# Optimization experiments

Measured on AMD Instinct MI355X. Metric: run time of the kernel, lower is better.

## Reference

```python
import jax, jax.numpy as jnp
import numpy as np

N_USER = 100000
N_ITEM = 100000
N_EDGE = 1600000
HID = 64
IN_U = 128
IN_I = 64
N_LAYERS = 2


def setup_inputs() -> dict:
    key = jax.random.key(0)
    ks = jax.random.split(key, 12)
    s = 0.05
    return {
        "x_user": jax.random.normal(ks[0], (N_USER, IN_U), jnp.float32),
        "x_item": jax.random.normal(ks[1], (N_ITEM, IN_I), jnp.float32),
        "edge_ui": jax.random.randint(ks[2], (2, N_EDGE), 0, N_USER),  # row0 src(user), row1 dst(item)
        "edge_iu": jax.random.randint(ks[3], (2, N_EDGE), 0, N_ITEM),  # row0 src(item), row1 dst(user)
        "Wu": jax.random.normal(ks[4], (IN_U, HID), jnp.float32) * s,
        "bu": jnp.zeros((HID,), jnp.float32),
        "Wi": jax.random.normal(ks[5], (IN_I, HID), jnp.float32) * s,
        "bi": jnp.zeros((HID,), jnp.float32),
        "Wl": jax.random.normal(ks[6], (N_LAYERS, 2, HID, HID), jnp.float32) * s,
        "bl": jnp.zeros((N_LAYERS, 2, HID), jnp.float32),
        "Wr": jax.random.normal(ks[7], (N_LAYERS, 2, HID, HID), jnp.float32) * s,
    }


def _sage(h_src, h_dst, edge, Wl, bl, Wr, n_dst):
    # SAGEConv: mean-aggregate gathered source features, then lin_l(agg)+bias + lin_r(dst)
    src, dst = edge[0], edge[1]
    msg = h_src[src]  # [E, HID] gather
    agg = jax.ops.segment_sum(msg, dst, num_segments=n_dst)
    cnt = jax.ops.segment_sum(jnp.ones((edge.shape[1], 1), h_src.dtype), dst, num_segments=n_dst)
    mean = agg / jnp.maximum(cnt, 1.0)
    return mean @ Wl + bl + h_dst @ Wr


def reference(x_user, x_item, edge_ui, edge_iu, Wu, bu, Wi, bi, Wl, bl, Wr):
    # per-node-type input linear + relu (dropout = identity at inference)
    hu = jax.nn.relu(x_user @ Wu + bu)
    hi = jax.nn.relu(x_item @ Wi + bi)
    for l in range(N_LAYERS):
        # edge type 0: user -> item ; edge type 1: item -> user ; HeteroConv aggr='sum'
        new_i = _sage(hu, hi, edge_ui, Wl[l, 0], bl[l, 0], Wr[l, 0], N_ITEM)
        new_u = _sage(hi, hu, edge_iu, Wl[l, 1], bl[l, 1], Wr[l, 1], N_USER)
        hu = jax.nn.relu(new_u)
        hi = jax.nn.relu(new_i)
    return hu, hi
```

## Files before the change

### kernel.cpp

```cpp
#include <hip/hip_runtime.h>

#define NUSER 100000
#define NITEM 100000
#define NEDGE 1600000
#define HID 64
#define NPB 256
#define NBKT 391
#define BCAP 5120
#define ACHUNK 8192
#define NCHUNK ((NEDGE + ACHUNK - 1) / ACHUNK)

typedef float f32x4 __attribute__((ext_vector_type(4)));

__device__ __forceinline__ unsigned short f2bf(float x) {
  unsigned int u; __builtin_memcpy(&u, &x, 4);
  u += 0x7fffu + ((u >> 16) & 1u);
  return (unsigned short)(u >> 16);
}
__device__ __forceinline__ float bflo(unsigned int u) {
  unsigned int v = u << 16; float f; __builtin_memcpy(&f, &v, 4); return f;
}
__device__ __forceinline__ float bfhi(unsigned int u) {
  unsigned int v = u & 0xffff0000u; float f; __builtin_memcpy(&f, &v, 4); return f;
}

__global__ __launch_bounds__(256) void gemm_in2(
    const float* __restrict__ A0, const float* __restrict__ W0,
    const float* __restrict__ bias0, float* __restrict__ C0,
    const float* __restrict__ A1, const float* __restrict__ W1,
    const float* __restrict__ bias1, float* __restrict__ C1, int M)
{
  __shared__ float Ws[128 * 64];
  __shared__ float As[64 * 68];
  const int tid = threadIdx.x;

  const int side = blockIdx.x & 1;
  const int t0 = blockIdx.x >> 1;
  const int nb = gridDim.x >> 1;
  const float* A; const float* W; const float* bias; float* C; int K;
  if (side == 0) { A = A0; W = W0; bias = bias0; C = C0; K = 128; }
  else           { A = A1; W = W1; bias = bias1; C = C1; K = 64; }

  for (int i = tid; i < K * 16; i += 256)
    ((float4*)Ws)[i] = ((const float4*)W)[i];

  const int tx = tid & 15;
  const int ty = tid >> 4;
  float4 bv = ((const float4*)bias)[tx];

  const int ntiles = (M + 63) >> 6;
  for (int t = t0; t < ntiles; t += nb) {
    const int row0 = t << 6;
    float acc[4][4] = {};
    for (int kb = 0; kb < K; kb += 64) {
      __syncthreads();
      for (int i = tid; i < 1024; i += 256) {
        int r = i >> 4;
        int kk = (i & 15) << 2;
        int gr = row0 + r; if (gr > M - 1) gr = M - 1;
        *(float4*)&As[r * 68 + kk] = *(const float4*)(A + (size_t)gr * K + kb + kk);
      }
      __syncthreads();
      #pragma unroll 8
      for (int k = 0; k < 64; ++k) {
        float4 w = *(const float4*)&Ws[(kb + k) * 64 + tx * 4];
        float a0 = As[(ty * 4 + 0) * 68 + k];
        float a1 = As[(ty * 4 + 1) * 68 + k];
        float a2 = As[(ty * 4 + 2) * 68 + k];
        float a3 = As[(ty * 4 + 3) * 68 + k];
        acc[0][0] += a0 * w.x; acc[0][1] += a0 * w.y; acc[0][2] += a0 * w.z; acc[0][3] += a0 * w.w;
        acc[1][0] += a1 * w.x; acc[1][1] += a1 * w.y; acc[1][2] += a1 * w.z; acc[1][3] += a1 * w.w;
        acc[2][0] += a2 * w.x; acc[2][1] += a2 * w.y; acc[2][2] += a2 * w.z; acc[2][3] += a2 * w.w;
        acc[3][0] += a3 * w.x; acc[3][1] += a3 * w.y; acc[3][2] += a3 * w.z; acc[3][3] += a3 * w.w;
      }
    }
    #pragma unroll
    for (int r = 0; r < 4; ++r) {
      int gr = row0 + ty * 4 + r;
      if (gr < M) {
        float4 o = make_float4(fmaxf(acc[r][0] + bv.x, 0.f), fmaxf(acc[r][1] + bv.y, 0.f),
                               fmaxf(acc[r][2] + bv.z, 0.f), fmaxf(acc[r][3] + bv.w, 0.f));
        *(float4*)(C + (size_t)gr * 64 + tx * 4) = o;
      }
    }
  }
}

__global__ __launch_bounds__(256) void gemm_dual2(
    const float* A0, const float* __restrict__ Wa0, const float* __restrict__ Wb0,
    const float* __restrict__ bias0, unsigned short* Ga0, float* Tb0,
    const float* A1, const float* __restrict__ Wa1, const float* __restrict__ Wb1,
    const float* __restrict__ bias1, unsigned short* Ga1, float* Tb1,
    int M)
{
  __shared__ float Ws[64 * 128];
  __shared__ float As[64 * 68];
  const int tid = threadIdx.x;
  const int half = gridDim.x >> 1;

  const float* A; const float* Wa; const float* Wb; const float* bias;
  unsigned short* Ga; float* Tb; int t0;
  if ((int)blockIdx.x < half) {
    A = A0; Wa = Wa0; Wb = Wb0; bias = bias0; Ga = Ga0; Tb = Tb0; t0 = blockIdx.x;
  } else {
    A = A1; Wa = Wa1; Wb = Wb1; bias = bias1; Ga = Ga1; Tb = Tb1; t0 = blockIdx.x - half;
  }

  for (int i = tid; i < 2048; i += 256) {
    int k = i >> 5, cg = i & 31;
    float4 v = (cg < 16) ? ((const float4*)Wa)[k * 16 + cg]
                         : ((const float4*)Wb)[k * 16 + (cg - 16)];
    ((float4*)Ws)[k * 32 + cg] = v;
  }

  const int tx = tid & 15;
  const int ty = tid >> 4;
  float4 bvB = ((const float4*)bias)[tx];

  const int ntiles = (M + 63) >> 6;
  for (int t = t0; t < ntiles; t += half) {
    const int row0 = t << 6;
    float accA[4][4] = {};
    float accB[4][4] = {};
    __syncthreads();
    for (int i = tid; i < 1024; i += 256) {
      int r = i >> 4;
      int kk = (i & 15) << 2;
      int gr = row0 + r; if (gr > M - 1) gr = M - 1;
      *(float4*)&As[r * 68 + kk] = *(const float4*)(A + (size_t)gr * 64 + kk);
    }
    __syncthreads();
    #pragma unroll 8
    for (int k = 0; k < 64; ++k) {
      float4 wa = *(const float4*)&Ws[k * 128 + tx * 4];
      float4 wb = *(const float4*)&Ws[k * 128 + 64 + tx * 4];
      float a0 = As[(ty * 4 + 0) * 68 + k];
      float a1 = As[(ty * 4 + 1) * 68 + k];
      float a2 = As[(ty * 4 + 2) * 68 + k];
      float a3 = As[(ty * 4 + 3) * 68 + k];
      accA[0][0] += a0 * wa.x; accA[0][1] += a0 * wa.y; accA[0][2] += a0 * wa.z; accA[0][3] += a0 * wa.w;
      accA[1][0] += a1 * wa.x; accA[1][1] += a1 * wa.y; accA[1][2] += a1 * wa.z; accA[1][3] += a1 * wa.w;
      accA[2][0] += a2 * wa.x; accA[2][1] += a2 * wa.y; accA[2][2] += a2 * wa.z; accA[2][3] += a2 * wa.w;
      accA[3][0] += a3 * wa.x; accA[3][1] += a3 * wa.y; accA[3][2] += a3 * wa.z; accA[3][3] += a3 * wa.w;
      accB[0][0] += a0 * wb.x; accB[0][1] += a0 * wb.y; accB[0][2] += a0 * wb.z; accB[0][3] += a0 * wb.w;
      accB[1][0] += a1 * wb.x; accB[1][1] += a1 * wb.y; accB[1][2] += a1 * wb.z; accB[1][3] += a1 * wb.w;
      accB[2][0] += a2 * wb.x; accB[2][1] += a2 * wb.y; accB[2][2] += a2 * wb.z; accB[2][3] += a2 * wb.w;
      accB[3][0] += a3 * wb.x; accB[3][1] += a3 * wb.y; accB[3][2] += a3 * wb.z; accB[3][3] += a3 * wb.w;
    }
    #pragma unroll
    for (int r = 0; r < 4; ++r) {
      int gr = row0 + ty * 4 + r;
      if (gr < M) {
        ushort4 g;
        g.x = f2bf(accA[r][0]); g.y = f2bf(accA[r][1]);
        g.z = f2bf(accA[r][2]); g.w = f2bf(accA[r][3]);
        *(ushort4*)(Ga + (size_t)gr * 64 + tx * 4) = g;
        *(float4*)(Tb + (size_t)gr * 64 + tx * 4) =
            make_float4(accB[r][0] + bvB.x, accB[r][1] + bvB.y,
                        accB[r][2] + bvB.z, accB[r][3] + bvB.w);
      }
    }
  }
}

__global__ __launch_bounds__(256) void agg2(
    const unsigned short* __restrict__ G0, const float* T0,
    const int2* __restrict__ ptr0, const int* __restrict__ idx0, float* out0,
    const unsigned short* __restrict__ G1, const float* T1,
    const int2* __restrict__ ptr1, const int* __restrict__ idx1, float* out1,
    int n_dst)
{
  const int lane = threadIdx.x & 63;
  const int sub = lane >> 5;
  const int s32 = lane & 31;
  const int k = s32 >> 4;
  const int c4 = (s32 & 15) << 2;
  int wave = blockIdx.x * 4 + (threadIdx.x >> 6);
  const int nwh = (gridDim.x * 4) >> 1;
  const unsigned short* G; const float* T; const int2* ptr; const int* idx; float* out;
  if (wave < nwh) { G = G0; T = T0; ptr = ptr0; idx = idx0; out = out0; }
  else { G = G1; T = T1; ptr = ptr1; idx = idx1; out = out1; wave -= nwh; }

  for (int n0 = wave * 2; n0 < n_dst; n0 += nwh * 2) {
    const int n = n0 + sub;
    if (n >= n_dst) continue;
    const int2 pe = ptr[n];
    const int s = pe.x;
    const int e = pe.y;
    f32x4 t = {};
    if (k == 0)
      t = __builtin_nontemporal_load((const f32x4*)(T + (size_t)n * 64 + c4));
    float a0 = 0.f, a1 = 0.f, a2 = 0.f, a3 = 0.f;
    int i = s;
    for (; i + 16 <= e; i += 16) {
      int j0 = __builtin_nontemporal_load(idx + i + 0  + k);
      int j1 = __builtin_nontemporal_load(idx + i + 2  + k);
      int j2 = __builtin_nontemporal_load(idx + i + 4  + k);
      int j3 = __builtin_nontemporal_load(idx + i + 6  + k);
      int j4 = __builtin_nontemporal_load(idx + i + 8  + k);
      int j5 = __builtin_nontemporal_load(idx + i + 10 + k);
      int j6 = __builtin_nontemporal_load(idx + i + 12 + k);
      int j7 = __builtin_nontemporal_load(idx + i + 14 + k);
      uint2 g0 = *(const uint2*)(G + (size_t)j0 * 64 + c4);
      uint2 g1 = *(const uint2*)(G + (size_t)j1 * 64 + c4);
      uint2 g2 = *(const uint2*)(G + (size_t)j2 * 64 + c4);
      uint2 g3 = *(const uint2*)(G + (size_t)j3 * 64 + c4);
      uint2 g4 = *(const uint2*)(G + (size_t)j4 * 64 + c4);
      uint2 g5 = *(const uint2*)(G + (size_t)j5 * 64 + c4);
      uint2 g6 = *(const uint2*)(G + (size_t)j6 * 64 + c4);
      uint2 g7 = *(const uint2*)(G + (size_t)j7 * 64 + c4);
      a0 += bflo(g0.x); a1 += bfhi(g0.x); a2 += bflo(g0.y); a3 += bfhi(g0.y);
      a0 += bflo(g1.x); a1 += bfhi(g1.x); a2 += bflo(g1.y); a3 += bfhi(g1.y);
      a0 += bflo(g2.x); a1 += bfhi(g2.x); a2 += bflo(g2.y); a3 += bfhi(g2.y);
      a0 += bflo(g3.x); a1 += bfhi(g3.x); a2 += bflo(g3.y); a3 += bfhi(g3.y);
      a0 += bflo(g4.x); a1 += bfhi(g4.x); a2 += bflo(g4.y); a3 += bfhi(g4.y);
      a0 += bflo(g5.x); a1 += bfhi(g5.x); a2 += bflo(g5.y); a3 += bfhi(g5.y);
      a0 += bflo(g6.x); a1 += bfhi(g6.x); a2 += bflo(g6.y); a3 += bfhi(g6.y);
      a0 += bflo(g7.x); a1 += bfhi(g7.x); a2 += bflo(g7.y); a3 += bfhi(g7.y);
    }
    if (i < e) {
      const int em1 = e - 1;
      const int t0 = i + 0  + k, t1 = i + 2  + k, t2 = i + 4  + k, t3 = i + 6  + k;
      const int t4 = i + 8  + k, t5 = i + 10 + k, t6 = i + 12 + k, t7 = i + 14 + k;
      int j0 = __builtin_nontemporal_load(idx + min(t0, em1));
      int j1 = __builtin_nontemporal_load(idx + min(t1, em1));
      int j2 = __builtin_nontemporal_load(idx + min(t2, em1));
      int j3 = __builtin_nontemporal_load(idx + min(t3, em1));
      int j4 = __builtin_nontemporal_load(idx + min(t4, em1));
      int j5 = __builtin_nontemporal_load(idx + min(t5, em1));
      int j6 = __builtin_nontemporal_load(idx + min(t6, em1));
      int j7 = __builtin_nontemporal_load(idx + min(t7, em1));
      uint2 g0 = *(const uint2*)(G + (size_t)j0 * 64 + c4);
      uint2 g1 = *(const uint2*)(G + (size_t)j1 * 64 + c4);
      uint2 g2 = *(const uint2*)(G + (size_t)j2 * 64 + c4);
      uint2 g3 = *(const uint2*)(G + (size_t)j3 * 64 + c4);
      uint2 g4 = *(const uint2*)(G + (size_t)j4 * 64 + c4);
      uint2 g5 = *(const uint2*)(G + (size_t)j5 * 64 + c4);
      uint2 g6 = *(const uint2*)(G + (size_t)j6 * 64 + c4);
      uint2 g7 = *(const uint2*)(G + (size_t)j7 * 64 + c4);
      float w0 = (t0 <= em1) ? 1.f : 0.f;
      float w1 = (t1 <= em1) ? 1.f : 0.f;
      float w2 = (t2 <= em1) ? 1.f : 0.f;
      float w3 = (t3 <= em1) ? 1.f : 0.f;
      float w4 = (t4 <= em1) ? 1.f : 0.f;
      float w5 = (t5 <= em1) ? 1.f : 0.f;
      float w6 = (t6 <= em1) ? 1.f : 0.f;
      float w7 = (t7 <= em1) ? 1.f : 0.f;
      a0 = fmaf(bflo(g0.x), w0, a0); a1 = fmaf(bfhi(g0.x), w0, a1);
      a2 = fmaf(bflo(g0.y), w0, a2); a3 = fmaf(bfhi(g0.y), w0, a3);
      a0 = fmaf(bflo(g1.x), w1, a0); a1 = fmaf(bfhi(g1.x), w1, a1);
      a2 = fmaf(bflo(g1.y), w1, a2); a3 = fmaf(bfhi(g1.y), w1, a3);
      a0 = fmaf(bflo(g2.x), w2, a0); a1 = fmaf(bfhi(g2.x), w2, a1);
      a2 = fmaf(bflo(g2.y), w2, a2); a3 = fmaf(bfhi(g2.y), w2, a3);
      a0 = fmaf(bflo(g3.x), w3, a0); a1 = fmaf(bfhi(g3.x), w3, a1);
      a2 = fmaf(bflo(g3.y), w3, a2); a3 = fmaf(bfhi(g3.y), w3, a3);
      a0 = fmaf(bflo(g4.x), w4, a0); a1 = fmaf(bfhi(g4.x), w4, a1);
      a2 = fmaf(bflo(g4.y), w4, a2); a3 = fmaf(bfhi(g4.y), w4, a3);
      a0 = fmaf(bflo(g5.x), w5, a0); a1 = fmaf(bfhi(g5.x), w5, a1);
      a2 = fmaf(bflo(g5.y), w5, a2); a3 = fmaf(bfhi(g5.y), w5, a3);
      a0 = fmaf(bflo(g6.x), w6, a0); a1 = fmaf(bfhi(g6.x), w6, a1);
      a2 = fmaf(bflo(g6.y), w6, a2); a3 = fmaf(bfhi(g6.y), w6, a3);
      a0 = fmaf(bflo(g7.x), w7, a0); a1 = fmaf(bfhi(g7.x), w7, a1);
      a2 = fmaf(bflo(g7.y), w7, a2); a3 = fmaf(bfhi(g7.y), w7, a3);
    }
    a0 += __shfl_xor(a0, 16);
    a1 += __shfl_xor(a1, 16);
    a2 += __shfl_xor(a2, 16);
    a3 += __shfl_xor(a3, 16);
    const int deg = e - s;
    const float inv = 1.f / (float)(deg > 0 ? deg : 1);
    if (k == 0) {
      f32x4 o;
      o.x = fmaxf(fmaf(a0, inv, t.x), 0.f);
      o.y = fmaxf(fmaf(a1, inv, t.y), 0.f);
      o.z = fmaxf(fmaf(a2, inv, t.z), 0.f);
      o.w = fmaxf(fmaf(a3, inv, t.w), 0.f);
      __builtin_nontemporal_store(o, (f32x4*)(out + (size_t)n * 64 + c4));
    }
  }
}

__global__ __launch_bounds__(256) void partition2(
    const int* __restrict__ srcA, const int* __restrict__ dstA, int* curA, unsigned int* pairsA,
    const int* __restrict__ srcB, const int* __restrict__ dstB, int* curB, unsigned int* pairsB,
    int E)
{
  __shared__ int h[NBKT];
  __shared__ int c[NBKT];
  const int half = gridDim.x >> 1;
  const bool isB = (int)blockIdx.x >= half;
  const int chunk = isB ? blockIdx.x - half : blockIdx.x;
  const int* src = isB ? srcB : srcA;
  const int* dst = isB ? dstB : dstA;
  int* cur = isB ? curB : curA;
  unsigned int* pairs = isB ? pairsB : pairsA;
  const int e0 = chunk * ACHUNK;
  const int e1 = min(e0 + ACHUNK, E);
  for (int i = threadIdx.x; i < NBKT; i += 256) h[i] = 0;
  __syncthreads();
  for (int e = e0 + (int)threadIdx.x; e < e1; e += 256)
    atomicAdd(&h[__builtin_nontemporal_load(dst + e) >> 8], 1);
  __syncthreads();
  for (int i = threadIdx.x; i < NBKT; i += 256) {
    int v = h[i];
    if (v) c[i] = i * BCAP + atomicAdd(&cur[i], v);
  }
  __syncthreads();
  for (int e = e0 + (int)threadIdx.x; e < e1; e += 256) {
    int d = __builtin_nontemporal_load(dst + e);
    int s = __builtin_nontemporal_load(src + e);
    int b = d >> 8;
    int p = atomicAdd(&c[b], 1);
    pairs[p] = ((unsigned int)(d & 255) << 24) | (unsigned int)s;
  }
}

__global__ __launch_bounds__(256) void bucket_fill(
    const unsigned int* __restrict__ pairsA, const int* __restrict__ cntA,
    int2* __restrict__ ptrA, int* __restrict__ idxA,
    const unsigned int* __restrict__ pairsB, const int* __restrict__ cntB,
    int2* __restrict__ ptrB, int* __restrict__ idxB, int n)
{
  __shared__ int h[NPB];
  __shared__ int cur[NPB];
  const bool isB = (int)blockIdx.x >= NBKT;
  const int b = isB ? blockIdx.x - NBKT : blockIdx.x;
  const unsigned int* pairs = isB ? pairsB : pairsA;
  const int* cnt = isB ? cntB : cntA;
  int2* ptr = isB ? ptrB : ptrA;
  int* idx = isB ? idxB : idxA;
  const int ebase = b * BCAP;
  const int eend = ebase + min(cnt[b], BCAP);
  const int t = threadIdx.x;
  h[t] = 0;
  __syncthreads();
  for (int e = ebase + t; e < eend; e += 256)
    atomicAdd(&h[pairs[e] >> 24], 1);
  __syncthreads();
  const int v = h[t];
  __syncthreads();
  for (int off = 1; off < 256; off <<= 1) {
    int x = 0;
    if (t >= off) x = h[t - off];
    __syncthreads();
    if (t >= off) h[t] += x;
    __syncthreads();
  }
  const int excl = h[t] - v;
  const int gnode = b * NPB + t;
  if (gnode < n) ptr[gnode] = make_int2(ebase + excl, ebase + excl + v);
  cur[t] = excl;
  __syncthreads();
  for (int e = ebase + t; e < eend; e += 256) {
    unsigned int pk = pairs[e];
    int p = atomicAdd(&cur[pk >> 24], 1);
    idx[ebase + p] = (int)(pk & 0xFFFFFFu);
  }
}

extern "C" void kernel_launch(void* const* d_in, const int* in_sizes, int n_in,
                              void* d_out, int out_size, void* d_ws, size_t ws_size,
                              hipStream_t stream) {
  const float* x_user = (const float*)d_in[0];
  const float* x_item = (const float*)d_in[1];
  const int*   edge_ui = (const int*)d_in[2];
  const int*   edge_iu = (const int*)d_in[3];
  const float* Wu = (const float*)d_in[4];
  const float* bu = (const float*)d_in[5];
  const float* Wi = (const float*)d_in[6];
  const float* bi = (const float*)d_in[7];
  const float* Wl = (const float*)d_in[8];
  const float* bl = (const float*)d_in[9];
  const float* Wr = (const float*)d_in[10];

  float* outU = (float*)d_out;
  float* outI = outU + (size_t)NUSER * HID;

  char* p = (char*)d_ws;
  auto alloc = [&](size_t bytes) -> void* {
    void* r = (void*)p; p += (bytes + 255) & ~(size_t)255; return r;
  };
  float* U = (float*)alloc((size_t)NUSER * HID * 4);
  float* I = (float*)alloc((size_t)NITEM * HID * 4);
  unsigned short* GA = (unsigned short*)alloc((size_t)NUSER * HID * 2);
  unsigned short* GB = (unsigned short*)alloc((size_t)NITEM * HID * 2);
  unsigned int* pairsA = (unsigned int*)GA;
  unsigned int* pairsB = (unsigned int*)GB;
  int* curA = (int*)alloc((size_t)(2 * NBKT) * 4);
  int* curB = curA + NBKT;
  int2* ptr_ui = (int2*)alloc(((size_t)NITEM) * 8);
  int2* ptr_iu = (int2*)alloc(((size_t)NUSER) * 8);
  int* idx_ui = (int*)alloc((size_t)NBKT * BCAP * 4);
  int* idx_iu = (int*)alloc((size_t)NBKT * BCAP * 4);

  hipError_t _e = hipMemsetAsync(curA, 0, (size_t)(2 * NBKT) * 4, stream); (void)_e;
  partition2<<<2 * NCHUNK, 256, 0, stream>>>(
      edge_ui, edge_ui + NEDGE, curA, pairsA,
      edge_iu, edge_iu + NEDGE, curB, pairsB, NEDGE);
  bucket_fill<<<2 * NBKT, 256, 0, stream>>>(pairsA, curA, ptr_ui, idx_ui,
                                            pairsB, curB, ptr_iu, idx_iu, NITEM);

  const int AGG_B = 2 * ((NUSER / 2 + 3) / 4);

  const float* Wl00 = Wl;             const float* Wl01 = Wl + 4096;
  const float* Wl10 = Wl + 2 * 4096;  const float* Wl11 = Wl + 3 * 4096;
  const float* Wr00 = Wr;             const float* Wr01 = Wr + 4096;
  const float* Wr10 = Wr + 2 * 4096;  const float* Wr11 = Wr + 3 * 4096;
  const float* bl00 = bl;             const float* bl01 = bl + 64;
  const float* bl10 = bl + 128;       const float* bl11 = bl + 192;

  gemm_in2<<<1152, 256, 0, stream>>>(x_user, Wu, bu, U,
                                     x_item, Wi, bi, I, NUSER);

  gemm_dual2<<<1536, 256, 0, stream>>>(U, Wl00, Wr01, bl01, GA, outU,
                                       I, Wl01, Wr00, bl00, GB, outI,
                                       NUSER);
  agg2<<<AGG_B, 256, 0, stream>>>(GA, outI, ptr_ui, idx_ui, outI,
                                  GB, outU, ptr_iu, idx_iu, outU, NITEM);

  gemm_dual2<<<1536, 256, 0, stream>>>(outI, Wl11, Wr10, bl10, GA, outI,
                                       outU, Wl10, Wr11, bl11, GB, outU,
                                       NITEM);
  agg2<<<AGG_B, 256, 0, stream>>>(GA, outU, ptr_iu, idx_iu, outU,
                                  GB, outI, ptr_ui, idx_ui, outI, NUSER);
}
```

Before: 540.7 us.

## Merge graph-partition and bucket-fill kernels into GEMM launches via block-range dispatch

The edge partition kernel is merged into the input GEMM launch, and the bucket-fill kernel into the first dual GEMM launch. Each fused launch dispatches on block index, with shared memory unioned between the two roles. Because the pairs buffers previously aliased the GA/GB buffers that the dual GEMM writes, they now get their own workspace allocations. The aim is to cut launch count and let the independent CSR-building work overlap with the dense GEMMs, at the cost of extra workspace memory and larger shared-memory footprints for the small partition blocks.

```diff
diff --git a/kernel.cpp b/kernel.cpp
--- a/kernel.cpp
+++ b/kernel.cpp
@@ -24,25 +24,62 @@
   unsigned int v = u & 0xffff0000u; float f; __builtin_memcpy(&f, &v, 4); return f;
 }
 
-__global__ __launch_bounds__(256) void gemm_in2(
+__global__ __launch_bounds__(256) void fused_a(
+    const int* __restrict__ srcA, const int* __restrict__ dstA, int* curA, unsigned int* pairsA,
+    const int* __restrict__ srcB, const int* __restrict__ dstB, int* curB, unsigned int* pairsB,
+    int E,
     const float* __restrict__ A0, const float* __restrict__ W0,
     const float* __restrict__ bias0, float* __restrict__ C0,
     const float* __restrict__ A1, const float* __restrict__ W1,
-    const float* __restrict__ bias1, float* __restrict__ C1, int M)
+    const float* __restrict__ bias1, float* __restrict__ C1, int M,
+    int part_blocks)
 {
-  __shared__ float Ws[128 * 64];
-  __shared__ float As[64 * 68];
+  __shared__ union {
+    struct { float Ws[128 * 64]; float As[64 * 68]; } g;
+    struct { int h[NBKT]; int c[NBKT]; } p;
+  } sm;
   const int tid = threadIdx.x;
 
-  const int side = blockIdx.x & 1;
-  const int t0 = blockIdx.x >> 1;
-  const int nb = gridDim.x >> 1;
+  if ((int)blockIdx.x < part_blocks) {
+    const int half = part_blocks >> 1;
+    const bool isB = (int)blockIdx.x >= half;
+    const int chunk = isB ? blockIdx.x - half : blockIdx.x;
+    const int* src = isB ? srcB : srcA;
+    const int* dst = isB ? dstB : dstA;
+    int* cur = isB ? curB : curA;
+    unsigned int* pairs = isB ? pairsB : pairsA;
+    const int e0 = chunk * ACHUNK;
+    const int e1 = min(e0 + ACHUNK, E);
+    for (int i = tid; i < NBKT; i += 256) sm.p.h[i] = 0;
+    __syncthreads();
+    for (int e = e0 + tid; e < e1; e += 256)
+      atomicAdd(&sm.p.h[__builtin_nontemporal_load(dst + e) >> 8], 1);
+    __syncthreads();
+    for (int i = tid; i < NBKT; i += 256) {
+      int v = sm.p.h[i];
+      if (v) sm.p.c[i] = i * BCAP + atomicAdd(&cur[i], v);
+    }
+    __syncthreads();
+    for (int e = e0 + tid; e < e1; e += 256) {
+      int d = __builtin_nontemporal_load(dst + e);
+      int s = __builtin_nontemporal_load(src + e);
+      int b = d >> 8;
+      int p = atomicAdd(&sm.p.c[b], 1);
+      pairs[p] = ((unsigned int)(d & 255) << 24) | (unsigned int)s;
+    }
+    return;
+  }
+
+  const int gb = blockIdx.x - part_blocks;
+  const int side = gb & 1;
+  const int t0 = gb >> 1;
+  const int nb = (gridDim.x - part_blocks) >> 1;
   const float* A; const float* W; const float* bias; float* C; int K;
   if (side == 0) { A = A0; W = W0; bias = bias0; C = C0; K = 128; }
   else           { A = A1; W = W1; bias = bias1; C = C1; K = 64; }
 
   for (int i = tid; i < K * 16; i += 256)
-    ((float4*)Ws)[i] = ((const float4*)W)[i];
+    ((float4*)sm.g.Ws)[i] = ((const float4*)W)[i];
 
   const int tx = tid & 15;
   const int ty = tid >> 4;
@@ -58,16 +95,16 @@
         int r = i >> 4;
         int kk = (i & 15) << 2;
         int gr = row0 + r; if (gr > M - 1) gr = M - 1;
-        *(float4*)&As[r * 68 + kk] = *(const float4*)(A + (size_t)gr * K + kb + kk);
+        *(float4*)&sm.g.As[r * 68 + kk] = *(const float4*)(A + (size_t)gr * K + kb + kk);
       }
       __syncthreads();
       #pragma unroll 8
       for (int k = 0; k < 64; ++k) {
-        float4 w = *(const float4*)&Ws[(kb + k) * 64 + tx * 4];
-        float a0 = As[(ty * 4 + 0) * 68 + k];
-        float a1 = As[(ty * 4 + 1) * 68 + k];
-        float a2 = As[(ty * 4 + 2) * 68 + k];
-        float a3 = As[(ty * 4 + 3) * 68 + k];
+        float4 w = *(const float4*)&sm.g.Ws[(kb + k) * 64 + tx * 4];
+        float a0 = sm.g.As[(ty * 4 + 0) * 68 + k];
+        float a1 = sm.g.As[(ty * 4 + 1) * 68 + k];
+        float a2 = sm.g.As[(ty * 4 + 2) * 68 + k];
+        float a3 = sm.g.As[(ty * 4 + 3) * 68 + k];
         acc[0][0] += a0 * w.x; acc[0][1] += a0 * w.y; acc[0][2] += a0 * w.z; acc[0][3] += a0 * w.w;
         acc[1][0] += a1 * w.x; acc[1][1] += a1 * w.y; acc[1][2] += a1 * w.z; acc[1][3] += a1 * w.w;
         acc[2][0] += a2 * w.x; acc[2][1] += a2 * w.y; acc[2][2] += a2 * w.z; acc[2][3] += a2 * w.w;
@@ -81,6 +118,127 @@
         float4 o = make_float4(fmaxf(acc[r][0] + bv.x, 0.f), fmaxf(acc[r][1] + bv.y, 0.f),
                                fmaxf(acc[r][2] + bv.z, 0.f), fmaxf(acc[r][3] + bv.w, 0.f));
         *(float4*)(C + (size_t)gr * 64 + tx * 4) = o;
+      }
+    }
+  }
+}
+
+__global__ __launch_bounds__(256) void fused_b(
+    const unsigned int* __restrict__ pairsA, const int* __restrict__ cntA,
+    int2* __restrict__ ptrA, int* __restrict__ idxA,
+    const unsigned int* __restrict__ pairsB, const int* __restrict__ cntB,
+    int2* __restrict__ ptrB, int* __restrict__ idxB, int n,
+    const float* A0, const float* __restrict__ Wa0, const float* __restrict__ Wb0,
+    const float* __restrict__ bias0, unsigned short* Ga0, float* Tb0,
+    const float* A1, const float* __restrict__ Wa1, const float* __restrict__ Wb1,
+    const float* __restrict__ bias1, unsigned short* Ga1, float* Tb1,
+    int M, int fill_blocks)
+{
+  __shared__ union {
+    struct { float Ws[64 * 128]; float As[64 * 68]; } g;
+    struct { int h[NPB]; int cur[NPB]; } f;
+  } sm;
+  const int tid = threadIdx.x;
+
+  if ((int)blockIdx.x < fill_blocks) {
+    const bool isB = (int)blockIdx.x >= NBKT;
+    const int b = isB ? blockIdx.x - NBKT : blockIdx.x;
+    const unsigned int* pairs = isB ? pairsB : pairsA;
+    const int* cnt = isB ? cntB : cntA;
+    int2* ptr = isB ? ptrB : ptrA;
+    int* idx = isB ? idxB : idxA;
+    const int ebase = b * BCAP;
+    const int eend = ebase + min(cnt[b], BCAP);
+    const int t = tid;
+    sm.f.h[t] = 0;
+    __syncthreads();
+    for (int e = ebase + t; e < eend; e += 256)
+      atomicAdd(&sm.f.h[pairs[e] >> 24], 1);
+    __syncthreads();
+    const int v = sm.f.h[t];
+    __syncthreads();
+    for (int off = 1; off < 256; off <<= 1) {
+      int x = 0;
+      if (t >= off) x = sm.f.h[t - off];
+      __syncthreads();
+      if (t >= off) sm.f.h[t] += x;
+      __syncthreads();
+    }
+    const int excl = sm.f.h[t] - v;
+    const int gnode = b * NPB + t;
+    if (gnode < n) ptr[gnode] = make_int2(ebase + excl, ebase + excl + v);
+    sm.f.cur[t] = excl;
+    __syncthreads();
+    for (int e = ebase + t; e < eend; e += 256) {
+      unsigned int pk = pairs[e];
+      int p = atomicAdd(&sm.f.cur[pk >> 24], 1);
+      idx[ebase + p] = (int)(pk & 0xFFFFFFu);
+    }
+    return;
+  }
+
+  const int gb = blockIdx.x - fill_blocks;
+  const int half = (gridDim.x - fill_blocks) >> 1;
+  const float* A; const float* Wa; const float* Wb; const float* bias;
+  unsigned short* Ga; float* Tb; int t0;
+  if (gb < half) {
+    A = A0; Wa = Wa0; Wb = Wb0; bias = bias0; Ga = Ga0; Tb = Tb0; t0 = gb;
+  } else {
+    A = A1; Wa = Wa1; Wb = Wb1; bias = bias1; Ga = Ga1; Tb = Tb1; t0 = gb - half;
+  }
+
+  for (int i = tid; i < 2048; i += 256) {
+    int k = i >> 5, cg = i & 31;
+    float4 v = (cg < 16) ? ((const float4*)Wa)[k * 16 + cg]
+                         : ((const float4*)Wb)[k * 16 + (cg - 16)];
+    ((float4*)sm.g.Ws)[k * 32 + cg] = v;
+  }
+
+  const int tx = tid & 15;
+  const int ty = tid >> 4;
+  float4 bvB = ((const float4*)bias)[tx];
+
+  const int ntiles = (M + 63) >> 6;
+  for (int t = t0; t < ntiles; t += half) {
+    const int row0 = t << 6;
+    float accA[4][4] = {};
+    float accB[4][4] = {};
+    __syncthreads();
+    for (int i = tid; i < 1024; i += 256) {
+      int r = i >> 4;
+      int kk = (i & 15) << 2;
+      int gr = row0 + r; if (gr > M - 1) gr = M - 1;
+      *(float4*)&sm.g.As[r * 68 + kk] = *(const float4*)(A + (size_t)gr * 64 + kk);
+    }
+    __syncthreads();
+    #pragma unroll 8
+    for (int k = 0; k < 64; ++k) {
+      float4 wa = *(const float4*)&sm.g.Ws[k * 128 + tx * 4];
+      float4 wb = *(const float4*)&sm.g.Ws[k * 128 + 64 + tx * 4];
+      float a0 = sm.g.As[(ty * 4 + 0) * 68 + k];
+      float a1 = sm.g.As[(ty * 4 + 1) * 68 + k];
+      float a2 = sm.g.As[(ty * 4 + 2) * 68 + k];
+      float a3 = sm.g.As[(ty * 4 + 3) * 68 + k];
+      accA[0][0] += a0 * wa.x; accA[0][1] += a0 * wa.y; accA[0][2] += a0 * wa.z; accA[0][3] += a0 * wa.w;
+      accA[1][0] += a1 * wa.x; accA[1][1] += a1 * wa.y; accA[1][2] += a1 * wa.z; accA[1][3] += a1 * wa.w;
+      accA[2][0] += a2 * wa.x; accA[2][1] += a2 * wa.y; accA[2][2] += a2 * wa.z; accA[2][3] += a2 * wa.w;
+      accA[3][0] += a3 * wa.x; accA[3][1] += a3 * wa.y; accA[3][2] += a3 * wa.z; accA[3][3] += a3 * wa.w;
+      accB[0][0] += a0 * wb.x; accB[0][1] += a0 * wb.y; accB[0][2] += a0 * wb.z; accB[0][3] += a0 * wb.w;
+      accB[1][0] += a1 * wb.x; accB[1][1] += a1 * wb.y; accB[1][2] += a1 * wb.z; accB[1][3] += a1 * wb.w;
+      accB[2][0] += a2 * wb.x; accB[2][1] += a2 * wb.y; accB[2][2] += a2 * wb.z; accB[2][3] += a2 * wb.w;
+      accB[3][0] += a3 * wb.x; accB[3][1] += a3 * wb.y; accB[3][2] += a3 * wb.z; accB[3][3] += a3 * wb.w;
+    }
+    #pragma unroll
+    for (int r = 0; r < 4; ++r) {
+      int gr = row0 + ty * 4 + r;
+      if (gr < M) {
+        ushort4 g;
+        g.x = f2bf(accA[r][0]); g.y = f2bf(accA[r][1]);
+        g.z = f2bf(accA[r][2]); g.w = f2bf(accA[r][3]);
+        *(ushort4*)(Ga + (size_t)gr * 64 + tx * 4) = g;
+        *(float4*)(Tb + (size_t)gr * 64 + tx * 4) =
+            make_float4(accB[r][0] + bvB.x, accB[r][1] + bvB.y,
+                        accB[r][2] + bvB.z, accB[r][3] + bvB.w);
       }
     }
   }
@@ -280,84 +438,6 @@
   }
 }
 
-__global__ __launch_bounds__(256) void partition2(
-    const int* __restrict__ srcA, const int* __restrict__ dstA, int* curA, unsigned int* pairsA,
-    const int* __restrict__ srcB, const int* __restrict__ dstB, int* curB, unsigned int* pairsB,
-    int E)
-{
-  __shared__ int h[NBKT];
-  __shared__ int c[NBKT];
-  const int half = gridDim.x >> 1;
-  const bool isB = (int)blockIdx.x >= half;
-  const int chunk = isB ? blockIdx.x - half : blockIdx.x;
-  const int* src = isB ? srcB : srcA;
-  const int* dst = isB ? dstB : dstA;
-  int* cur = isB ? curB : curA;
-  unsigned int* pairs = isB ? pairsB : pairsA;
-  const int e0 = chunk * ACHUNK;
-  const int e1 = min(e0 + ACHUNK, E);
-  for (int i = threadIdx.x; i < NBKT; i += 256) h[i] = 0;
-  __syncthreads();
-  for (int e = e0 + (int)threadIdx.x; e < e1; e += 256)
-    atomicAdd(&h[__builtin_nontemporal_load(dst + e) >> 8], 1);
-  __syncthreads();
-  for (int i = threadIdx.x; i < NBKT; i += 256) {
-    int v = h[i];
-    if (v) c[i] = i * BCAP + atomicAdd(&cur[i], v);
-  }
-  __syncthreads();
-  for (int e = e0 + (int)threadIdx.x; e < e1; e += 256) {
-    int d = __builtin_nontemporal_load(dst + e);
-    int s = __builtin_nontemporal_load(src + e);
-    int b = d >> 8;
-    int p = atomicAdd(&c[b], 1);
-    pairs[p] = ((unsigned int)(d & 255) << 24) | (unsigned int)s;
-  }
-}
-
-__global__ __launch_bounds__(256) void bucket_fill(
-    const unsigned int* __restrict__ pairsA, const int* __restrict__ cntA,
-    int2* __restrict__ ptrA, int* __restrict__ idxA,
-    const unsigned int* __restrict__ pairsB, const int* __restrict__ cntB,
-    int2* __restrict__ ptrB, int* __restrict__ idxB, int n)
-{
-  __shared__ int h[NPB];
-  __shared__ int cur[NPB];
-  const bool isB = (int)blockIdx.x >= NBKT;
-  const int b = isB ? blockIdx.x - NBKT : blockIdx.x;
-  const unsigned int* pairs = isB ? pairsB : pairsA;
-  const int* cnt = isB ? cntB : cntA;
-  int2* ptr = isB ? ptrB : ptrA;
-  int* idx = isB ? idxB : idxA;
-  const int ebase = b * BCAP;
-  const int eend = ebase + min(cnt[b], BCAP);
-  const int t = threadIdx.x;
-  h[t] = 0;
-  __syncthreads();
-  for (int e = ebase + t; e < eend; e += 256)
-    atomicAdd(&h[pairs[e] >> 24], 1);
-  __syncthreads();
-  const int v = h[t];
-  __syncthreads();
-  for (int off = 1; off < 256; off <<= 1) {
-    int x = 0;
-    if (t >= off) x = h[t - off];
-    __syncthreads();
-    if (t >= off) h[t] += x;
-    __syncthreads();
-  }
-  const int excl = h[t] - v;
-  const int gnode = b * NPB + t;
-  if (gnode < n) ptr[gnode] = make_int2(ebase + excl, ebase + excl + v);
-  cur[t] = excl;
-  __syncthreads();
-  for (int e = ebase + t; e < eend; e += 256) {
-    unsigned int pk = pairs[e];
-    int p = atomicAdd(&cur[pk >> 24], 1);
-    idx[ebase + p] = (int)(pk & 0xFFFFFFu);
-  }
-}
-
 extern "C" void kernel_launch(void* const* d_in, const int* in_sizes, int n_in,
                               void* d_out, int out_size, void* d_ws, size_t ws_size,
                               hipStream_t stream) {
@@ -384,8 +464,8 @@
   float* I = (float*)alloc((size_t)NITEM * HID * 4);
   unsigned short* GA = (unsigned short*)alloc((size_t)NUSER * HID * 2);
   unsigned short* GB = (unsigned short*)alloc((size_t)NITEM * HID * 2);
-  unsigned int* pairsA = (unsigned int*)GA;
-  unsigned int* pairsB = (unsigned int*)GB;
+  unsigned int* pairsA = (unsigned int*)alloc((size_t)NBKT * BCAP * 4);
+  unsigned int* pairsB = (unsigned int*)alloc((size_t)NBKT * BCAP * 4);
   int* curA = (int*)alloc((size_t)(2 * NBKT) * 4);
   int* curB = curA + NBKT;
   int2* ptr_ui = (int2*)alloc(((size_t)NITEM) * 8);
@@ -394,11 +474,6 @@
   int* idx_iu = (int*)alloc((size_t)NBKT * BCAP * 4);
 
   hipError_t _e = hipMemsetAsync(curA, 0, (size_t)(2 * NBKT) * 4, stream); (void)_e;
-  partition2<<<2 * NCHUNK, 256, 0, stream>>>(
-      edge_ui, edge_ui + NEDGE, curA, pairsA,
-      edge_iu, edge_iu + NEDGE, curB, pairsB, NEDGE);
-  bucket_fill<<<2 * NBKT, 256, 0, stream>>>(pairsA, curA, ptr_ui, idx_ui,
-                                            pairsB, curB, ptr_iu, idx_iu, NITEM);
 
   const int AGG_B = 2 * ((NUSER / 2 + 3) / 4);
 
@@ -409,18 +484,27 @@
   const float* bl00 = bl;             const float* bl01 = bl + 64;
   const float* bl10 = bl + 128;       const float* bl11 = bl + 192;
 
-  gemm_in2<<<1152, 256, 0, stream>>>(x_user, Wu, bu, U,
-                                     x_item, Wi, bi, I, NUSER);
-
-  gemm_dual2<<<1536, 256, 0, stream>>>(U, Wl00, Wr01, bl01, GA, outU,
-                                       I, Wl01, Wr00, bl00, GB, outI,
-                                       NUSER);
+  fused_a<<<2 * NCHUNK + 1152, 256, 0, stream>>>(
+      edge_ui, edge_ui + NEDGE, curA, pairsA,
+      edge_iu, edge_iu + NEDGE, curB, pairsB, NEDGE,
+      x_user, Wu, bu, U,
+      x_item, Wi, bi, I, NUSER,
+      2 * NCHUNK);
+
+  fused_b<<<2 * NBKT + 1536, 256, 0, stream>>>(
+      pairsA, curA, ptr_ui, idx_ui,
+      pairsB, curB, ptr_iu, idx_iu, NITEM,
+      U, Wl00, Wr01, bl01, GA, outU,
+      I, Wl01, Wr00, bl00, GB, outI,
+      NUSER, 2 * NBKT);
+
   agg2<<<AGG_B, 256, 0, stream>>>(GA, outI, ptr_ui, idx_ui, outI,
                                   GB, outU, ptr_iu, idx_iu, outU, NITEM);
 
   gemm_dual2<<<1536, 256, 0, stream>>>(outI, Wl11, Wr10, bl10, GA, outI,
                                        outU, Wl10, Wr11, bl11, GB, outU,
                                        NITEM);
+
   agg2<<<AGG_B, 256, 0, stream>>>(GA, outU, ptr_iu, idx_iu, outU,
                                   GB, outI, ptr_ui, idx_ui, outI, NUSER);
 }
```

New measurement: 566.2 us. 1.05x slower.
